# Performance work log

Hardware: AMD Instinct MI355X
Metric: run time of the kernel (lower is better)

Reference implementation:

```python
import jax, jax.numpy as jnp
import numpy as np

N = 40000          # nodes
E = 640000         # edges (avg degree 16)
D = 128            # in_channels == out_channels
G = 8              # graphs
NPG = N // G       # nodes per graph
EPS = 1e-6
SLOPE = 0.01       # torch LeakyReLU default


def leaky(x):
    return jnp.where(x >= 0, x, SLOPE * x)


def setup_inputs() -> dict:
    key = jax.random.key(0)
    ks = jax.random.split(key, 8)
    x = jax.random.normal(ks[0], (N, D), dtype=jnp.float32)
    edge_index = jax.random.randint(ks[1], (2, E), 0, N, dtype=jnp.int32)
    w = jax.random.uniform(ks[2], (E, 1), dtype=jnp.float32)
    batch = jnp.repeat(jnp.arange(G, dtype=jnp.int32), NPG)
    batch_num = jnp.full((G,), NPG, dtype=jnp.int32)
    s = 1.0 / np.sqrt(D)
    W1 = jax.random.uniform(ks[3], (D, D), jnp.float32, -s, s)
    W2 = jax.random.uniform(ks[4], (D, D), jnp.float32, -s, s)
    Wo = jax.random.uniform(ks[5], (D, D), jnp.float32, -s, s)
    Wn = jax.random.uniform(ks[6], (D, D), jnp.float32, -s, s)
    gamma = jnp.ones((D,), jnp.float32)
    beta = jnp.zeros((D,), jnp.float32)
    return {"x": x, "edge_index": edge_index, "w": w, "batch": batch,
            "batch_num": batch_num, "W1": W1, "W2": W2, "Wo": Wo, "Wn": Wn,
            "gamma": gamma, "beta": beta}


def reference(x, edge_index, w, batch, batch_num, W1, W2, Wo, Wn, gamma, beta):
    # mlp_x (dropout in eval mode => identity)
    h = leaky(x @ W1) @ W2                                    # [N, D]
    # gather -> scale -> scatter-sum -> activate
    xj = w * h[edge_index[1]]                                 # [E, D]
    xn = leaky(jax.ops.segment_sum(xj, edge_index[0], num_segments=N))
    out = h @ Wo + xn @ Wn                                    # [N, D]
    # GraphNorm: per-graph mean and unbiased std (torch_scatter defaults)
    cnt = batch_num.astype(jnp.float32)[:, None]              # [G, 1]
    mu = jax.ops.segment_sum(out, batch, num_segments=G) / cnt
    diff = out - mu[batch]
    var = jax.ops.segment_sum(diff * diff, batch, num_segments=G) / (cnt - 1.0)
    sigma = jnp.sqrt(var)
    return diff / (sigma[batch] + EPS) * gamma + beta
```

## Files before the change

### kernel.cpp

```cpp
#include <hip/hip_runtime.h>
#include <hip/hip_bf16.h>

#define D 128
#define NN 40000
#define EE 640000
#define GG 8
#define NPG 5000
#define CAP 32
#define OVCAP 4096

using short8 = __attribute__((ext_vector_type(8))) short;
using f32x4 = __attribute__((ext_vector_type(4))) float;

__device__ __forceinline__ float lrelu(float v) { return v >= 0.f ? v : 0.01f * v; }

__device__ __forceinline__ ushort f2bf(float f) {
    union { float f; uint u; } c; c.f = f;
    return (ushort)((c.u + 0x7FFFu + ((c.u >> 16) & 1u)) >> 16);
}
__device__ __forceinline__ float bf2f_lo(uint u) { union { uint u; float f; } c; c.u = u << 16; return c.f; }
__device__ __forceinline__ float bf2f_hi(uint u) { union { uint u; float f; } c; c.u = u & 0xFFFF0000u; return c.f; }

__global__ __launch_bounds__(256) void wtrans_k(const float* __restrict__ W1,
                                                const float* __restrict__ W2,
                                                const float* __restrict__ Wo,
                                                const float* __restrict__ Wn,
                                                short* __restrict__ WT) {
    const float* W = blockIdx.x == 0 ? W1 : blockIdx.x == 1 ? W2 : blockIdx.x == 2 ? Wo : Wn;
    short* T = WT + blockIdx.x * (D * D);
#pragma unroll 4
    for (int i = 0; i < 64; ++i) {
        int flat = threadIdx.x + i * 256;
        int k = flat >> 7, n = flat & 127;
        T[n * D + k] = (short)f2bf(W[flat]);
    }
}

__device__ __forceinline__ void stage_B(const short* __restrict__ WT,
                                        short (*Bs)[136], int tid) {
    const uint4* bsrc = (const uint4*)WT;
#pragma unroll
    for (int i = 0; i < 8; ++i) {
        int idx = tid + i * 256;
        int flat = idx * 8;
        *(uint4*)&Bs[flat >> 7][flat & 127] = bsrc[idx];
    }
}

template <int ABF, int LKA>
__device__ __forceinline__ void stage_A(const void* __restrict__ Av,
                                        short (*As)[136], int arow, int tid) {
    if constexpr (ABF) {
        const uint4* asrc = (const uint4*)Av;
#pragma unroll
        for (int i = 0; i < 4; ++i) {
            int idx = tid + i * 256;
            int flat = idx * 8;
            *(uint4*)&As[flat >> 7][flat & 127] = asrc[(size_t)arow * 16 + idx];
        }
    } else {
        const float4* A4 = (const float4*)Av;
#pragma unroll
        for (int i = 0; i < 8; ++i) {
            int idx = tid + i * 256;
            int row = idx >> 5, kq = idx & 31;
            float4 v = A4[(size_t)(arow + row) * 32 + kq];
            if (LKA) { v.x = lrelu(v.x); v.y = lrelu(v.y); v.z = lrelu(v.z); v.w = lrelu(v.w); }
            uint2 p;
            p.x = (uint)f2bf(v.x) | ((uint)f2bf(v.y) << 16);
            p.y = (uint)f2bf(v.z) | ((uint)f2bf(v.w) << 16);
            *(uint2*)&As[row][kq * 4] = p;
        }
    }
}

__device__ __forceinline__ void do_mfma(short (*As)[136], short (*Bs)[136],
                                        f32x4 (&acc)[8], int tid) {
    const int lane = tid & 63;
    const int m0 = (tid >> 6) * 16;
    const int lrow = lane & 15;
    const int kgrp = (lane >> 4) * 8;
#pragma unroll
    for (int ks = 0; ks < 4; ++ks) {
        const int kb = ks * 32 + kgrp;
        short8 a = *(const short8*)&As[m0 + lrow][kb];
#pragma unroll
        for (int nt = 0; nt < 8; ++nt) {
            short8 b = *(const short8*)&Bs[nt * 16 + lrow][kb];
            acc[nt] = __builtin_amdgcn_mfma_f32_16x16x32_bf16(a, b, acc[nt], 0, 0, 0);
        }
    }
}

__global__ __launch_bounds__(256) void mlp_k(const float* __restrict__ x,
                                             const short* __restrict__ W1T,
                                             const short* __restrict__ W2T,
                                             ushort* __restrict__ h) {
    __shared__ short As[64][136];
    __shared__ short Bs[128][136];
    const int tid = threadIdx.x;
    const int arow = blockIdx.x * 64;
    f32x4 acc[8] = {};
    stage_A<0, 0>(x, As, arow, tid);
    stage_B(W1T, Bs, tid);
    __syncthreads();
    do_mfma(As, Bs, acc, tid);
    __syncthreads();
    const int lane = tid & 63;
    const int c0 = lane & 15;
    const int r0 = (tid >> 6) * 16 + ((lane >> 4) << 2);
#pragma unroll
    for (int nt = 0; nt < 8; ++nt)
#pragma unroll
        for (int r = 0; r < 4; ++r)
            As[r0 + r][nt * 16 + c0] = (short)f2bf(lrelu(acc[nt][r]));
    stage_B(W2T, Bs, tid);
#pragma unroll
    for (int nt = 0; nt < 8; ++nt) acc[nt] = f32x4{0.f, 0.f, 0.f, 0.f};
    __syncthreads();
    do_mfma(As, Bs, acc, tid);
#pragma unroll
    for (int nt = 0; nt < 8; ++nt)
#pragma unroll
        for (int r = 0; r < 4; ++r)
            h[(size_t)(arow + r0 + r) * D + nt * 16 + c0] = f2bf(acc[nt][r]);
}

template <int A1BF, int LK1, int TWO, int A2BF, int LK2, int LKOUT, int CBF>
__global__ __launch_bounds__(256) void mm_k(const void* __restrict__ A1,
                                            const short* __restrict__ WT1,
                                            const void* __restrict__ A2,
                                            const short* __restrict__ WT2,
                                            void* __restrict__ Cv) {
    __shared__ short As[64][136];
    __shared__ short Bs[128][136];
    const int tid = threadIdx.x;
    const int arow = blockIdx.x * 64;
    f32x4 acc[8] = {};
    stage_A<A1BF, LK1>(A1, As, arow, tid);
    stage_B(WT1, Bs, tid);
    __syncthreads();
    do_mfma(As, Bs, acc, tid);
    __syncthreads();
    if constexpr (TWO) {
        stage_A<A2BF, LK2>(A2, As, arow, tid);
        stage_B(WT2, Bs, tid);
        __syncthreads();
        do_mfma(As, Bs, acc, tid);
        __syncthreads();
    }
    const int lane = tid & 63;
    const int c0 = lane & 15;
    const int r0 = (tid >> 6) * 16 + ((lane >> 4) << 2);
#pragma unroll
    for (int nt = 0; nt < 8; ++nt) {
#pragma unroll
        for (int r = 0; r < 4; ++r) {
            float v = acc[nt][r];
            if (LKOUT) v = lrelu(v);
            const size_t off = (size_t)(arow + r0 + r) * D + nt * 16 + c0;
            if constexpr (CBF) ((ushort*)Cv)[off] = f2bf(v);
            else ((float*)Cv)[off] = v;
        }
    }
}

__global__ __launch_bounds__(256) void fill_k(const int* __restrict__ ei,
                                              const float* __restrict__ w,
                                              int* __restrict__ deg,
                                              int2* __restrict__ csr,
                                              int* __restrict__ ov) {
    const int t = blockIdx.x * 256 + threadIdx.x;
    const int e0 = t * 4;
    const int4 dst = *(const int4*)&ei[e0];
    const int4 src = *(const int4*)&ei[EE + e0];
    const float4 wv = *(const float4*)&w[e0];
    int pos[4];
    pos[0] = atomicAdd(&deg[dst.x], 1);
    pos[1] = atomicAdd(&deg[dst.y], 1);
    pos[2] = atomicAdd(&deg[dst.z], 1);
    pos[3] = atomicAdd(&deg[dst.w], 1);
    const int ds[4] = {dst.x, dst.y, dst.z, dst.w};
    const int sr[4] = {src.x, src.y, src.z, src.w};
    const float wf[4] = {wv.x, wv.y, wv.z, wv.w};
#pragma unroll
    for (int t4 = 0; t4 < 4; ++t4) {
        if (pos[t4] < CAP) {
            csr[ds[t4] * CAP + pos[t4]] = make_int2(sr[t4], __float_as_int(wf[t4]));
        } else {
            const int oi = atomicAdd(&ov[0], 1);
            if (oi < OVCAP) ov[1 + oi] = e0 + t4;
        }
    }
}

__global__ __launch_bounds__(256) void gather_k(const ushort* __restrict__ h,
                                                const int* __restrict__ deg,
                                                const int2* __restrict__ csr,
                                                float* __restrict__ xn) {
    const int n = blockIdx.x * 8 + (threadIdx.x >> 5);
    const int lane = threadIdx.x & 31;
    int dn = deg[n];
    if (dn > CAP) dn = CAP;
    const int2* row = csr + (size_t)n * CAP;
    float4 acc = {0.f, 0.f, 0.f, 0.f};
    int j = 0;
    for (; j + 8 <= dn; j += 8) {
        int2 p[8]; uint2 v[8];
#pragma unroll
        for (int t = 0; t < 8; ++t) p[t] = row[j + t];
#pragma unroll
        for (int t = 0; t < 8; ++t) v[t] = *((const uint2*)(h + (size_t)p[t].x * D) + lane);
#pragma unroll
        for (int t = 0; t < 8; ++t) {
            const float wv = __int_as_float(p[t].y);
            acc.x += wv * bf2f_lo(v[t].x);
            acc.y += wv * bf2f_hi(v[t].x);
            acc.z += wv * bf2f_lo(v[t].y);
            acc.w += wv * bf2f_hi(v[t].y);
        }
    }
    if (j + 4 <= dn) {
        int2 p[4]; uint2 v[4];
#pragma unroll
        for (int t = 0; t < 4; ++t) p[t] = row[j + t];
#pragma unroll
        for (int t = 0; t < 4; ++t) v[t] = *((const uint2*)(h + (size_t)p[t].x * D) + lane);
#pragma unroll
        for (int t = 0; t < 4; ++t) {
            const float wv = __int_as_float(p[t].y);
            acc.x += wv * bf2f_lo(v[t].x);
            acc.y += wv * bf2f_hi(v[t].x);
            acc.z += wv * bf2f_lo(v[t].y);
            acc.w += wv * bf2f_hi(v[t].y);
        }
        j += 4;
    }
    for (; j < dn; ++j) {
        int2 p = row[j];
        const uint2 v = *((const uint2*)(h + (size_t)p.x * D) + lane);
        const float wv = __int_as_float(p.y);
        acc.x += wv * bf2f_lo(v.x);
        acc.y += wv * bf2f_hi(v.x);
        acc.z += wv * bf2f_lo(v.y);
        acc.w += wv * bf2f_hi(v.y);
    }
    *((float4*)(xn + (size_t)n * D) + lane) = acc;
}

__global__ __launch_bounds__(256) void overflow_k(const ushort* __restrict__ h,
                                                  const int* __restrict__ ei,
                                                  const float* __restrict__ w,
                                                  const int* __restrict__ ov,
                                                  float* __restrict__ xn) {
    int cnt = ov[0];
    if (cnt > OVCAP) cnt = OVCAP;
    const int wid = threadIdx.x >> 6;
    const int lane = threadIdx.x & 63;
    for (int i = wid; i < cnt; i += 4) {
        const int e = ov[1 + i];
        const int dst = ei[e];
        const int src = ei[EE + e];
        const float we = w[e];
        const uint v = *((const uint*)(h + (size_t)src * D) + lane);
        float* xr = xn + (size_t)dst * D + lane * 2;
        atomicAdd(xr, bf2f_lo(v) * we);
        atomicAdd(xr + 1, bf2f_hi(v) * we);
    }
}

__global__ __launch_bounds__(256) void stats_k(const float* __restrict__ out,
                                               float* __restrict__ stats) {
    const int g = blockIdx.x / 50, chunk = blockIdx.x % 50;
    const int d = threadIdx.x & 127, half = threadIdx.x >> 7;
    size_t base = ((size_t)g * NPG + chunk * 100) * D + d;
    float s = 0.f, ss = 0.f;
#pragma unroll 4
    for (int r = half; r < 100; r += 2) {
        float v = out[base + (size_t)r * D];
        s += v; ss += v * v;
    }
    atomicAdd(&stats[g * D + d], s);
    atomicAdd(&stats[GG * D + g * D + d], ss);
}

__global__ __launch_bounds__(256) void norm_k(float* __restrict__ out,
                                              const float* __restrict__ stats,
                                              const float* __restrict__ gamma,
                                              const float* __restrict__ beta) {
    const int i4 = blockIdx.x * 256 + threadIdx.x;
    const int row = i4 >> 5;
    const int g = row / NPG;
    const int d0 = (i4 & 31) * 4;
    float4 v = *((float4*)out + i4);
    const float4 s4 = *(const float4*)&stats[g * D + d0];
    const float4 q4 = *(const float4*)&stats[GG * D + g * D + d0];
    const float4 g4 = *(const float4*)&gamma[d0];
    const float4 b4 = *(const float4*)&beta[d0];
    const float inv = 1.f / (float)NPG;
    const float invm1 = 1.f / (float)(NPG - 1);
    float mu, var, sg;
    mu = s4.x * inv; var = (q4.x - s4.x * mu) * invm1; sg = sqrtf(fmaxf(var, 0.f));
    v.x = (v.x - mu) / (sg + 1e-6f) * g4.x + b4.x;
    mu = s4.y * inv; var = (q4.y - s4.y * mu) * invm1; sg = sqrtf(fmaxf(var, 0.f));
    v.y = (v.y - mu) / (sg + 1e-6f) * g4.y + b4.y;
    mu = s4.z * inv; var = (q4.z - s4.z * mu) * invm1; sg = sqrtf(fmaxf(var, 0.f));
    v.z = (v.z - mu) / (sg + 1e-6f) * g4.z + b4.z;
    mu = s4.w * inv; var = (q4.w - s4.w * mu) * invm1; sg = sqrtf(fmaxf(var, 0.f));
    v.w = (v.w - mu) / (sg + 1e-6f) * g4.w + b4.w;
    *((float4*)out + i4) = v;
}

extern "C" void kernel_launch(void* const* d_in, const int* in_sizes, int n_in,
                              void* d_out, int out_size, void* d_ws, size_t ws_size,
                              hipStream_t stream) {
    const float* x = (const float*)d_in[0];
    const int* ei = (const int*)d_in[1];
    const float* w = (const float*)d_in[2];
    const float* W1 = (const float*)d_in[5];
    const float* W2 = (const float*)d_in[6];
    const float* Wo = (const float*)d_in[7];
    const float* Wn = (const float*)d_in[8];
    const float* gamma = (const float*)d_in[9];
    const float* beta = (const float*)d_in[10];
    float* out = (float*)d_out;

    char* ws = (char*)d_ws;
    const size_t BF16MAT = (size_t)NN * D * 2;
    const size_t F32MAT = (size_t)NN * D * 4;
    size_t off = 0;
    ushort* h = (ushort*)(ws + off);   off += BF16MAT;
    float* xn = (float*)(ws + off);    off += F32MAT;
    float* stats = (float*)(ws + off); off += 2 * GG * D * 4 + 256;
    short* WT = (short*)(ws + off);    off += 4 * (size_t)D * D * 2;
    int* deg = (int*)(ws + off);       off += (size_t)NN * 4;
    int* ov = (int*)(ws + off);        off += (1 + OVCAP) * 4 + 252; off &= ~(size_t)255;
    int2* csr = (int2*)(ws + off);

    const int MM_GRID = NN / 64;

    wtrans_k<<<4, 256, 0, stream>>>(W1, W2, Wo, Wn, WT);
    mlp_k<<<MM_GRID, 256, 0, stream>>>(x, WT, WT + D * D, h);
    hipMemsetAsync(deg, 0, (size_t)NN * 4, stream);
    hipMemsetAsync(ov, 0, (1 + OVCAP) * 4, stream);
    hipMemsetAsync(stats, 0, 2 * GG * D * 4, stream);
    fill_k<<<EE / (256 * 4), 256, 0, stream>>>(ei, w, deg, csr, ov);
    gather_k<<<NN / 8, 256, 0, stream>>>(h, deg, csr, xn);
    overflow_k<<<1, 256, 0, stream>>>(h, ei, w, ov, xn);
    mm_k<1, 0, 1, 0, 1, 0, 0><<<MM_GRID, 256, 0, stream>>>(h, WT + 2 * D * D, xn, WT + 3 * D * D, out);
    stats_k<<<GG * 50, 256, 0, stream>>>(out, stats);
    norm_k<<<(NN * D / 4) / 256, 256, 0, stream>>>(out, stats, gamma, beta);
}
```

Measured before the change: 214.0 us.

## Fuse zeroing, overflow, activation and stats into neighbouring kernels; split degree counters

Folds the three memsets into the weight-transpose kernel and moves overflow-edge handling into the gather kernel, which now scans the overflow list only for nodes whose degree exceeds capacity. The gather applies LeakyReLU and writes bf16 instead of fp32, which halves that intermediate's traffic and lets the second GEMM load it directly. The GraphNorm sum and sum-of-squares are computed in the GEMM epilogue, with atomics spread over 8 replicas, so the separate stats pass over the output is removed. The per-node degree counter is split into two sub-counters with 16 slots each to reduce atomic contention. The costs are extra bf16 rounding on the aggregated features, a linear scan of the overflow list for high-degree nodes, and norm_k now summing 8 replicas.

```diff
diff --git a/kernel.cpp b/kernel.cpp
--- a/kernel.cpp
+++ b/kernel.cpp
@@ -6,8 +6,8 @@
 #define EE 640000
 #define GG 8
 #define NPG 5000
-#define CAP 32
-#define OVCAP 4096
+#define CSUB 16
+#define OVCAP 4095
 
 using short8 = __attribute__((ext_vector_type(8))) short;
 using f32x4 = __attribute__((ext_vector_type(4))) float;
@@ -21,18 +21,25 @@
 __device__ __forceinline__ float bf2f_lo(uint u) { union { uint u; float f; } c; c.u = u << 16; return c.f; }
 __device__ __forceinline__ float bf2f_hi(uint u) { union { uint u; float f; } c; c.u = u & 0xFFFF0000u; return c.f; }
 
-__global__ __launch_bounds__(256) void wtrans_k(const float* __restrict__ W1,
-                                                const float* __restrict__ W2,
-                                                const float* __restrict__ Wo,
-                                                const float* __restrict__ Wn,
-                                                short* __restrict__ WT) {
-    const float* W = blockIdx.x == 0 ? W1 : blockIdx.x == 1 ? W2 : blockIdx.x == 2 ? Wo : Wn;
-    short* T = WT + blockIdx.x * (D * D);
+__global__ __launch_bounds__(256) void prep_k(const float* __restrict__ W1,
+                                              const float* __restrict__ W2,
+                                              const float* __restrict__ Wo,
+                                              const float* __restrict__ Wn,
+                                              short* __restrict__ WT,
+                                              uint4* __restrict__ zbase, int zlen16) {
+    const int b = blockIdx.x;
+    if (b < 4) {
+        const float* W = b == 0 ? W1 : b == 1 ? W2 : b == 2 ? Wo : Wn;
+        short* T = WT + b * (D * D);
 #pragma unroll 4
-    for (int i = 0; i < 64; ++i) {
-        int flat = threadIdx.x + i * 256;
-        int k = flat >> 7, n = flat & 127;
-        T[n * D + k] = (short)f2bf(W[flat]);
+        for (int i = 0; i < 64; ++i) {
+            int flat = threadIdx.x + i * 256;
+            int k = flat >> 7, n = flat & 127;
+            T[n * D + k] = (short)f2bf(W[flat]);
+        }
+    } else {
+        int idx = (b - 4) * 256 + threadIdx.x;
+        if (idx < zlen16) zbase[idx] = uint4{0, 0, 0, 0};
     }
 }
 
@@ -47,7 +54,7 @@
     }
 }
 
-template <int ABF, int LKA>
+template <int ABF>
 __device__ __forceinline__ void stage_A(const void* __restrict__ Av,
                                         short (*As)[136], int arow, int tid) {
     if constexpr (ABF) {
@@ -65,7 +72,6 @@
             int idx = tid + i * 256;
             int row = idx >> 5, kq = idx & 31;
             float4 v = A4[(size_t)(arow + row) * 32 + kq];
-            if (LKA) { v.x = lrelu(v.x); v.y = lrelu(v.y); v.z = lrelu(v.z); v.w = lrelu(v.w); }
             uint2 p;
             p.x = (uint)f2bf(v.x) | ((uint)f2bf(v.y) << 16);
             p.y = (uint)f2bf(v.z) | ((uint)f2bf(v.w) << 16);
@@ -101,7 +107,7 @@
     const int tid = threadIdx.x;
     const int arow = blockIdx.x * 64;
     f32x4 acc[8] = {};
-    stage_A<0, 0>(x, As, arow, tid);
+    stage_A<0>(x, As, arow, tid);
     stage_B(W1T, Bs, tid);
     __syncthreads();
     do_mfma(As, Bs, acc, tid);
@@ -126,89 +132,44 @@
             h[(size_t)(arow + r0 + r) * D + nt * 16 + c0] = f2bf(acc[nt][r]);
 }
 
-template <int A1BF, int LK1, int TWO, int A2BF, int LK2, int LKOUT, int CBF>
-__global__ __launch_bounds__(256) void mm_k(const void* __restrict__ A1,
-                                            const short* __restrict__ WT1,
-                                            const void* __restrict__ A2,
-                                            const short* __restrict__ WT2,
-                                            void* __restrict__ Cv) {
-    __shared__ short As[64][136];
-    __shared__ short Bs[128][136];
-    const int tid = threadIdx.x;
-    const int arow = blockIdx.x * 64;
-    f32x4 acc[8] = {};
-    stage_A<A1BF, LK1>(A1, As, arow, tid);
-    stage_B(WT1, Bs, tid);
-    __syncthreads();
-    do_mfma(As, Bs, acc, tid);
-    __syncthreads();
-    if constexpr (TWO) {
-        stage_A<A2BF, LK2>(A2, As, arow, tid);
-        stage_B(WT2, Bs, tid);
-        __syncthreads();
-        do_mfma(As, Bs, acc, tid);
-        __syncthreads();
-    }
-    const int lane = tid & 63;
-    const int c0 = lane & 15;
-    const int r0 = (tid >> 6) * 16 + ((lane >> 4) << 2);
-#pragma unroll
-    for (int nt = 0; nt < 8; ++nt) {
-#pragma unroll
-        for (int r = 0; r < 4; ++r) {
-            float v = acc[nt][r];
-            if (LKOUT) v = lrelu(v);
-            const size_t off = (size_t)(arow + r0 + r) * D + nt * 16 + c0;
-            if constexpr (CBF) ((ushort*)Cv)[off] = f2bf(v);
-            else ((float*)Cv)[off] = v;
-        }
-    }
-}
-
 __global__ __launch_bounds__(256) void fill_k(const int* __restrict__ ei,
                                               const float* __restrict__ w,
-                                              int* __restrict__ deg,
+                                              int* __restrict__ deg2,
                                               int2* __restrict__ csr,
                                               int* __restrict__ ov) {
     const int t = blockIdx.x * 256 + threadIdx.x;
-    const int e0 = t * 4;
-    const int4 dst = *(const int4*)&ei[e0];
-    const int4 src = *(const int4*)&ei[EE + e0];
-    const float4 wv = *(const float4*)&w[e0];
-    int pos[4];
-    pos[0] = atomicAdd(&deg[dst.x], 1);
-    pos[1] = atomicAdd(&deg[dst.y], 1);
-    pos[2] = atomicAdd(&deg[dst.z], 1);
-    pos[3] = atomicAdd(&deg[dst.w], 1);
-    const int ds[4] = {dst.x, dst.y, dst.z, dst.w};
-    const int sr[4] = {src.x, src.y, src.z, src.w};
-    const float wf[4] = {wv.x, wv.y, wv.z, wv.w};
-#pragma unroll
-    for (int t4 = 0; t4 < 4; ++t4) {
-        if (pos[t4] < CAP) {
-            csr[ds[t4] * CAP + pos[t4]] = make_int2(sr[t4], __float_as_int(wf[t4]));
-        } else {
-            const int oi = atomicAdd(&ov[0], 1);
-            if (oi < OVCAP) ov[1 + oi] = e0 + t4;
-        }
-    }
+    const int e0 = t * 2;
+    const int2 dst = *(const int2*)&ei[e0];
+    const int2 src = *(const int2*)&ei[EE + e0];
+    const float2 wv = *(const float2*)&w[e0];
+    const int p0 = atomicAdd(&deg2[dst.x * 2], 1);
+    const int p1 = atomicAdd(&deg2[dst.y * 2 + 1], 1);
+    if (p0 < CSUB) csr[(size_t)dst.x * 32 + p0] = make_int2(src.x, __float_as_int(wv.x));
+    else { int oi = atomicAdd(&ov[0], 1); if (oi < OVCAP) ov[1 + oi] = e0; }
+    if (p1 < CSUB) csr[(size_t)dst.y * 32 + CSUB + p1] = make_int2(src.y, __float_as_int(wv.y));
+    else { int oi = atomicAdd(&ov[0], 1); if (oi < OVCAP) ov[1 + oi] = e0 + 1; }
 }
 
 __global__ __launch_bounds__(256) void gather_k(const ushort* __restrict__ h,
-                                                const int* __restrict__ deg,
+                                                const int* __restrict__ deg2,
                                                 const int2* __restrict__ csr,
-                                                float* __restrict__ xn) {
+                                                const int* __restrict__ ei,
+                                                const float* __restrict__ w,
+                                                const int* __restrict__ ov,
+                                                ushort* __restrict__ xnact) {
     const int n = blockIdx.x * 8 + (threadIdx.x >> 5);
     const int lane = threadIdx.x & 31;
-    int dn = deg[n];
-    if (dn > CAP) dn = CAP;
-    const int2* row = csr + (size_t)n * CAP;
+    const int2 dd = *(const int2*)&deg2[2 * n];
+    const int c0 = min(dd.x, CSUB), c1 = min(dd.y, CSUB);
+    const int total = c0 + c1;
+    const int shift = CSUB - c0;
+    const int2* row = csr + (size_t)n * 32;
     float4 acc = {0.f, 0.f, 0.f, 0.f};
     int j = 0;
-    for (; j + 8 <= dn; j += 8) {
+    for (; j + 8 <= total; j += 8) {
         int2 p[8]; uint2 v[8];
 #pragma unroll
-        for (int t = 0; t < 8; ++t) p[t] = row[j + t];
+        for (int t = 0; t < 8; ++t) { int jj = j + t; p[t] = row[jj < c0 ? jj : jj + shift]; }
 #pragma unroll
         for (int t = 0; t < 8; ++t) v[t] = *((const uint2*)(h + (size_t)p[t].x * D) + lane);
 #pragma unroll
@@ -220,10 +181,10 @@
             acc.w += wv * bf2f_hi(v[t].y);
         }
     }
-    if (j + 4 <= dn) {
+    if (j + 4 <= total) {
         int2 p[4]; uint2 v[4];
 #pragma unroll
-        for (int t = 0; t < 4; ++t) p[t] = row[j + t];
+        for (int t = 0; t < 4; ++t) { int jj = j + t; p[t] = row[jj < c0 ? jj : jj + shift]; }
 #pragma unroll
         for (int t = 0; t < 4; ++t) v[t] = *((const uint2*)(h + (size_t)p[t].x * D) + lane);
 #pragma unroll
@@ -236,8 +197,8 @@
         }
         j += 4;
     }
-    for (; j < dn; ++j) {
-        int2 p = row[j];
+    for (; j < total; ++j) {
+        int2 p = row[j < c0 ? j : j + shift];
         const uint2 v = *((const uint2*)(h + (size_t)p.x * D) + lane);
         const float wv = __int_as_float(p.y);
         acc.x += wv * bf2f_lo(v.x);
@@ -245,43 +206,84 @@
         acc.z += wv * bf2f_lo(v.y);
         acc.w += wv * bf2f_hi(v.y);
     }
-    *((float4*)(xn + (size_t)n * D) + lane) = acc;
-}
-
-__global__ __launch_bounds__(256) void overflow_k(const ushort* __restrict__ h,
-                                                  const int* __restrict__ ei,
-                                                  const float* __restrict__ w,
-                                                  const int* __restrict__ ov,
-                                                  float* __restrict__ xn) {
-    int cnt = ov[0];
-    if (cnt > OVCAP) cnt = OVCAP;
-    const int wid = threadIdx.x >> 6;
-    const int lane = threadIdx.x & 63;
-    for (int i = wid; i < cnt; i += 4) {
-        const int e = ov[1 + i];
-        const int dst = ei[e];
-        const int src = ei[EE + e];
-        const float we = w[e];
-        const uint v = *((const uint*)(h + (size_t)src * D) + lane);
-        float* xr = xn + (size_t)dst * D + lane * 2;
-        atomicAdd(xr, bf2f_lo(v) * we);
-        atomicAdd(xr + 1, bf2f_hi(v) * we);
-    }
-}
-
-__global__ __launch_bounds__(256) void stats_k(const float* __restrict__ out,
-                                               float* __restrict__ stats) {
-    const int g = blockIdx.x / 50, chunk = blockIdx.x % 50;
-    const int d = threadIdx.x & 127, half = threadIdx.x >> 7;
-    size_t base = ((size_t)g * NPG + chunk * 100) * D + d;
-    float s = 0.f, ss = 0.f;
-#pragma unroll 4
-    for (int r = half; r < 100; r += 2) {
-        float v = out[base + (size_t)r * D];
-        s += v; ss += v * v;
-    }
-    atomicAdd(&stats[g * D + d], s);
-    atomicAdd(&stats[GG * D + g * D + d], ss);
+    if (dd.x > CSUB || dd.y > CSUB) {
+        const int cnt = min(ov[0], OVCAP);
+        for (int i = 0; i < cnt; ++i) {
+            const int e = ov[1 + i];
+            if (ei[e] == n) {
+                const float wv = w[e];
+                const uint2 v = *((const uint2*)(h + (size_t)ei[EE + e] * D) + lane);
+                acc.x += wv * bf2f_lo(v.x);
+                acc.y += wv * bf2f_hi(v.x);
+                acc.z += wv * bf2f_lo(v.y);
+                acc.w += wv * bf2f_hi(v.y);
+            }
+        }
+    }
+    uint2 st;
+    st.x = (uint)f2bf(lrelu(acc.x)) | ((uint)f2bf(lrelu(acc.y)) << 16);
+    st.y = (uint)f2bf(lrelu(acc.z)) | ((uint)f2bf(lrelu(acc.w)) << 16);
+    *((uint2*)(xnact + (size_t)n * D) + lane) = st;
+}
+
+__global__ __launch_bounds__(256) void mmstats_k(const ushort* __restrict__ h,
+                                                 const short* __restrict__ WoT,
+                                                 const ushort* __restrict__ xa,
+                                                 const short* __restrict__ WnT,
+                                                 float* __restrict__ out,
+                                                 float* __restrict__ stats) {
+    __shared__ short As[64][136];
+    __shared__ short Bs[128][136];
+    const int tid = threadIdx.x;
+    const int arow = blockIdx.x * 64;
+    f32x4 acc[8] = {};
+    stage_A<1>(h, As, arow, tid);
+    stage_B(WoT, Bs, tid);
+    __syncthreads();
+    do_mfma(As, Bs, acc, tid);
+    __syncthreads();
+    stage_A<1>(xa, As, arow, tid);
+    stage_B(WnT, Bs, tid);
+    __syncthreads();
+    do_mfma(As, Bs, acc, tid);
+    __syncthreads();
+    float* ls_s = (float*)As;
+    float* ls_q = ls_s + 16 * 132;
+    const int lane = tid & 63;
+    const int c0 = lane & 15;
+    const int r0 = (tid >> 6) * 16 + ((lane >> 4) << 2);
+    const int li = (tid >> 6) * 4 + (lane >> 4);
+#pragma unroll
+    for (int nt = 0; nt < 8; ++nt) {
+        float s = 0.f, q = 0.f;
+#pragma unroll
+        for (int r = 0; r < 4; ++r) {
+            const float v = acc[nt][r];
+            out[(size_t)(arow + r0 + r) * D + nt * 16 + c0] = v;
+            s += v; q += v * v;
+        }
+        ls_s[li * 132 + nt * 16 + c0] = s;
+        ls_q[li * 132 + nt * 16 + c0] = q;
+    }
+    __syncthreads();
+    if (tid < 128) {
+        const int g0 = arow / NPG;
+        const int gsplit = (g0 + 1) * NPG - arow;
+        float s0 = 0.f, q0 = 0.f, s1 = 0.f, q1 = 0.f;
+#pragma unroll
+        for (int i = 0; i < 16; ++i) {
+            const float sv = ls_s[i * 132 + tid];
+            const float qv = ls_q[i * 132 + tid];
+            if (i * 4 >= gsplit) { s1 += sv; q1 += qv; }
+            else { s0 += sv; q0 += qv; }
+        }
+        const int rep = blockIdx.x & 7;
+        float* S = &stats[((size_t)(rep * 2 + 0) * GG + g0) * D + tid];
+        float* Q = &stats[((size_t)(rep * 2 + 1) * GG + g0) * D + tid];
+        atomicAdd(S, s0);
+        atomicAdd(Q, q0);
+        if (gsplit < 64) { atomicAdd(S + D, s1); atomicAdd(Q + D, q1); }
+    }
 }
 
 __global__ __launch_bounds__(256) void norm_k(float* __restrict__ out,
@@ -293,8 +295,14 @@
     const int g = row / NPG;
     const int d0 = (i4 & 31) * 4;
     float4 v = *((float4*)out + i4);
-    const float4 s4 = *(const float4*)&stats[g * D + d0];
-    const float4 q4 = *(const float4*)&stats[GG * D + g * D + d0];
+    float4 s4 = {0.f, 0.f, 0.f, 0.f}, q4 = {0.f, 0.f, 0.f, 0.f};
+#pragma unroll
+    for (int rep = 0; rep < 8; ++rep) {
+        const float4 sr = *(const float4*)&stats[((size_t)(rep * 2 + 0) * GG + g) * D + d0];
+        const float4 qr = *(const float4*)&stats[((size_t)(rep * 2 + 1) * GG + g) * D + d0];
+        s4.x += sr.x; s4.y += sr.y; s4.z += sr.z; s4.w += sr.w;
+        q4.x += qr.x; q4.y += qr.y; q4.z += qr.z; q4.w += qr.w;
+    }
     const float4 g4 = *(const float4*)&gamma[d0];
     const float4 b4 = *(const float4*)&beta[d0];
     const float inv = 1.f / (float)NPG;
@@ -327,27 +335,22 @@
 
     char* ws = (char*)d_ws;
     const size_t BF16MAT = (size_t)NN * D * 2;
-    const size_t F32MAT = (size_t)NN * D * 4;
     size_t off = 0;
-    ushort* h = (ushort*)(ws + off);   off += BF16MAT;
-    float* xn = (float*)(ws + off);    off += F32MAT;
-    float* stats = (float*)(ws + off); off += 2 * GG * D * 4 + 256;
-    short* WT = (short*)(ws + off);    off += 4 * (size_t)D * D * 2;
-    int* deg = (int*)(ws + off);       off += (size_t)NN * 4;
-    int* ov = (int*)(ws + off);        off += (1 + OVCAP) * 4 + 252; off &= ~(size_t)255;
+    ushort* h = (ushort*)(ws + off);      off += BF16MAT;
+    ushort* xnact = (ushort*)(ws + off);  off += BF16MAT;
+    const size_t ZOFF = off;
+    float* stats = (float*)(ws + off);    off += 8 * 2 * GG * D * 4;
+    int* deg2 = (int*)(ws + off);         off += (size_t)NN * 2 * 4;
+    int* ov = (int*)(ws + off);           off += (1 + OVCAP) * 4;
+    const int ZLEN16 = (int)((off - ZOFF) / 16);
+    short* WT = (short*)(ws + off);       off += 4 * (size_t)D * D * 2;
     int2* csr = (int2*)(ws + off);
 
-    const int MM_GRID = NN / 64;
-
-    wtrans_k<<<4, 256, 0, stream>>>(W1, W2, Wo, Wn, WT);
-    mlp_k<<<MM_GRID, 256, 0, stream>>>(x, WT, WT + D * D, h);
-    hipMemsetAsync(deg, 0, (size_t)NN * 4, stream);
-    hipMemsetAsync(ov, 0, (1 + OVCAP) * 4, stream);
-    hipMemsetAsync(stats, 0, 2 * GG * D * 4, stream);
-    fill_k<<<EE / (256 * 4), 256, 0, stream>>>(ei, w, deg, csr, ov);
-    gather_k<<<NN / 8, 256, 0, stream>>>(h, deg, csr, xn);
-    overflow_k<<<1, 256, 0, stream>>>(h, ei, w, ov, xn);
-    mm_k<1, 0, 1, 0, 1, 0, 0><<<MM_GRID, 256, 0, stream>>>(h, WT + 2 * D * D, xn, WT + 3 * D * D, out);
-    stats_k<<<GG * 50, 256, 0, stream>>>(out, stats);
+    prep_k<<<4 + (ZLEN16 + 255) / 256, 256, 0, stream>>>(W1, W2, Wo, Wn, WT,
+                                                         (uint4*)(ws + ZOFF), ZLEN16);
+    mlp_k<<<NN / 64, 256, 0, stream>>>(x, WT, WT + D * D, h);
+    fill_k<<<EE / (256 * 2), 256, 0, stream>>>(ei, w, deg2, csr, ov);
+    gather_k<<<NN / 8, 256, 0, stream>>>(h, deg2, csr, ei, w, ov, xnact);
+    mmstats_k<<<NN / 64, 256, 0, stream>>>(h, WT + 2 * D * D, xnact, WT + 3 * D * D, out, stats);
     norm_k<<<(NN * D / 4) / 256, 256, 0, stream>>>(out, stats, gamma, beta);
 }
```

After: 312.7 us. 46.1% more time.
